# Kernel optimization log

Measured on AMD Instinct MI355X. Metric: run time of the kernel, lower is better.

Reference implementation:

```python
import jax, jax.numpy as jnp
import numpy as np

N_NODES = 100000
N_EDGES = 1600000
D_IN = 128
HID = 32
HEADS = 4
D_OUT = 40
NEG_SLOPE = 0.2


def edge_softmax(scores, dst, n_nodes):
    # scores: [E, H]; softmax over incoming edges of each destination node
    m = jax.ops.segment_max(scores, dst, num_segments=n_nodes)  # [N, H]
    e = jnp.exp(scores - m[dst])
    s = jax.ops.segment_sum(e, dst, num_segments=n_nodes)  # [N, H]
    return e / s[dst]


def gat_conv(x, src, dst, W, attn_l, attn_r, bias):
    # x: [N, Din]; W: [Din, H*F]; attn_l/attn_r: [H, F]; bias: [H*F]
    n = x.shape[0]
    h = (x @ W).reshape(n, HEADS, HID)          # [N, H, F]
    el = jnp.einsum('nhf,hf->nh', h, attn_l)    # [N, H]
    er = jnp.einsum('nhf,hf->nh', h, attn_r)    # [N, H]
    e = jax.nn.leaky_relu(el[src] + er[dst], NEG_SLOPE)  # [E, H]
    a = edge_softmax(e, dst, n)                 # [E, H]
    msg = h[src] * a[:, :, None]                # [E, H, F]
    out = jax.ops.segment_sum(msg, dst, num_segments=n)  # [N, H, F]
    return out + bias.reshape(HEADS, HID)


def setup_inputs() -> dict:
    key = jax.random.key(0)
    ks = jax.random.split(key, 12)
    x = jax.random.normal(ks[0], (N_NODES, D_IN), dtype=jnp.float32)
    src = jax.random.randint(ks[1], (N_EDGES,), 0, N_NODES, dtype=jnp.int32)
    dst = jax.random.randint(ks[2], (N_EDGES,), 0, N_NODES, dtype=jnp.int32)
    s = 0.05
    W1 = jax.random.normal(ks[3], (D_IN, HEADS * HID), dtype=jnp.float32) * s
    al1 = jax.random.normal(ks[4], (HEADS, HID), dtype=jnp.float32) * s
    ar1 = jax.random.normal(ks[5], (HEADS, HID), dtype=jnp.float32) * s
    b1 = jnp.zeros((HEADS * HID,), dtype=jnp.float32)
    W2 = jax.random.normal(ks[6], (HEADS * HID, HEADS * HID), dtype=jnp.float32) * s
    al2 = jax.random.normal(ks[7], (HEADS, HID), dtype=jnp.float32) * s
    ar2 = jax.random.normal(ks[8], (HEADS, HID), dtype=jnp.float32) * s
    b2 = jnp.zeros((HEADS * HID,), dtype=jnp.float32)
    Wout = jax.random.normal(ks[9], (HEADS * HID, D_OUT), dtype=jnp.float32) * s
    bout = jnp.zeros((D_OUT,), dtype=jnp.float32)
    return {"x": x, "src": src, "dst": dst,
            "W1": W1, "al1": al1, "ar1": ar1, "b1": b1,
            "W2": W2, "al2": al2, "ar2": ar2, "b2": b2,
            "Wout": Wout, "bout": bout}


def reference(x, src, dst, W1, al1, ar1, b1, W2, al2, ar2, b2, Wout, bout):
    n = x.shape[0]
    h = gat_conv(x, src, dst, W1, al1, ar1, b1).reshape(n, -1)  # flatten(1)
    h = jax.nn.elu(h)
    h = gat_conv(h, src, dst, W2, al2, ar2, b2).reshape(n, -1)
    h = jax.nn.elu(h)
    return h @ Wout + bout  # final Linear, flatten(1) is a no-op on 2D
```

## Files before the change

kernel.cpp:

```cpp
#include <hip/hip_runtime.h>
#include <hip/hip_fp16.h>
#include <math.h>

#define N_NODES 100000
#define N_EDGES 1600000
#define NEG_SLOPE 0.2f

#define NB ((N_NODES + 255) / 256)
#define NC 1024
#define CHUNK ((N_EDGES + NC - 1) / NC)

__device__ __forceinline__ float lrelu(float x) { return x > 0.f ? x : NEG_SLOPE * x; }
__device__ __forceinline__ float eluf(float x)  { return x > 0.f ? x : expm1f(x); }


__global__ __launch_bounds__(256) void p1_hist(const int* __restrict__ dst,
                                               int* __restrict__ H) {
  __shared__ int hist[NB];
  int c = blockIdx.x, t = threadIdx.x;
  for (int i = t; i < NB; i += 256) hist[i] = 0;
  __syncthreads();
  int e0 = c * CHUNK, e1 = min(e0 + CHUNK, N_EDGES);
  for (int e = e0 + t; e < e1; e += 256) atomicAdd(&hist[dst[e] >> 8], 1);
  __syncthreads();
  for (int i = t; i < NB; i += 256) H[i * NC + c] = hist[i];
}

__global__ __launch_bounds__(256) void p2_colscan(int* __restrict__ H,
                                                  int* __restrict__ colTotal) {
  __shared__ int sh[256];
  int b = blockIdx.x, t = threadIdx.x;
  int4 v = *(int4*)&H[b * NC + t * 4];
  int tsum = v.x + v.y + v.z + v.w;
  sh[t] = tsum;
  __syncthreads();
  for (int off = 1; off < 256; off <<= 1) {
    int u = (t >= off) ? sh[t - off] : 0;
    __syncthreads();
    sh[t] += u;
    __syncthreads();
  }
  int excl = sh[t] - tsum;
  int4 o;
  o.x = excl;
  o.y = excl + v.x;
  o.z = o.y + v.y;
  o.w = o.z + v.z;
  *(int4*)&H[b * NC + t * 4] = o;
  if (t == 255) colTotal[b] = sh[255];
}

__global__ __launch_bounds__(512) void p3_bucketscan(const int* __restrict__ colTotal,
                                                     int* __restrict__ bucketBase) {
  __shared__ int sh[512];
  int t = threadIdx.x;
  int v = (t < NB) ? colTotal[t] : 0;
  sh[t] = v;
  __syncthreads();
  for (int off = 1; off < 512; off <<= 1) {
    int u = (t >= off) ? sh[t - off] : 0;
    __syncthreads();
    sh[t] += u;
    __syncthreads();
  }
  if (t < NB) bucketBase[t] = sh[t] - v;
  if (t == NB - 1) bucketBase[NB] = sh[t];
}

__global__ __launch_bounds__(256) void p4_scatter(const int* __restrict__ src,
                                                  const int* __restrict__ dst,
                                                  const int* __restrict__ H,
                                                  const int* __restrict__ bucketBase,
                                                  int* __restrict__ tmp) {
  __shared__ int cur[NB];
  int c = blockIdx.x, t = threadIdx.x;
  for (int i = t; i < NB; i += 256) cur[i] = bucketBase[i] + H[i * NC + c];
  __syncthreads();
  int e0 = c * CHUNK, e1 = min(e0 + CHUNK, N_EDGES);
  for (int e = e0 + t; e < e1; e += 256) {
    int d = dst[e];
    int pos = atomicAdd(&cur[d >> 8], 1);
    tmp[pos] = (src[e] << 8) | (d & 255);
  }
}

__global__ __launch_bounds__(256) void p5_build(const int* __restrict__ tmp,
                                                const int* __restrict__ bucketBase,
                                                int* __restrict__ rowstart,
                                                int* __restrict__ csr_src) {
  __shared__ int hist[256];
  __shared__ int sh[256];
  __shared__ int cur[256];
  int b = blockIdx.x, t = threadIdx.x;
  int ebase = bucketBase[b], eend = bucketBase[b + 1];
  hist[t] = 0;
  __syncthreads();
  for (int e = ebase + t; e < eend; e += 256) atomicAdd(&hist[tmp[e] & 255], 1);
  __syncthreads();
  int v = hist[t];
  sh[t] = v;
  __syncthreads();
  for (int off = 1; off < 256; off <<= 1) {
    int u = (t >= off) ? sh[t - off] : 0;
    __syncthreads();
    sh[t] += u;
    __syncthreads();
  }
  int excl = sh[t] - v;
  int node = b * 256 + t;
  if (node < N_NODES) rowstart[node] = ebase + excl;
  cur[t] = excl;
  __syncthreads();
  for (int e = ebase + t; e < eend; e += 256) {
    int p = tmp[e];
    int pos = ebase + atomicAdd(&cur[p & 255], 1);
    csr_src[pos] = p >> 8;
  }
  if (b == 0 && t == 0) rowstart[N_NODES] = N_EDGES;
}

template <bool FP16IN>
__global__ __launch_bounds__(256) void gemm128_elr(const void* __restrict__ Av,
                                                   const float* __restrict__ W,
                                                   const float* __restrict__ al,
                                                   const float* __restrict__ ar,
                                                   __half* __restrict__ C,
                                                   float* __restrict__ el,
                                                   float* __restrict__ er, int N) {
  __shared__ float As[32 * 68];
  __shared__ float Ws[32 * 132];
  __shared__ float als[128], ars[128];
  int tid = threadIdx.x;
  int tx = tid & 15, ty = tid >> 4;
  int rowBase = blockIdx.x * 64;

  if (tid < 128) { als[tid] = al[tid]; ars[tid] = ar[tid]; }

  float acc0[4][4] = {};
  float acc1[4][4] = {};

  const float4* W4 = (const float4*)W;

  for (int kc = 0; kc < 128; kc += 32) {
    __syncthreads();
    if constexpr (FP16IN) {
      const __half* A = (const __half*)Av;
      int r = tid >> 2, c8 = (tid & 3) * 8;
      int gr = min(rowBase + r, N - 1);
      float4 raw = *(const float4*)&A[(size_t)gr * 128 + kc + c8];
      const __half2* hp = (const __half2*)&raw;
      float2 f0 = __half22float2(hp[0]);
      float2 f1 = __half22float2(hp[1]);
      float2 f2 = __half22float2(hp[2]);
      float2 f3 = __half22float2(hp[3]);
      As[(c8 + 0) * 68 + r] = f0.x; As[(c8 + 1) * 68 + r] = f0.y;
      As[(c8 + 2) * 68 + r] = f1.x; As[(c8 + 3) * 68 + r] = f1.y;
      As[(c8 + 4) * 68 + r] = f2.x; As[(c8 + 5) * 68 + r] = f2.y;
      As[(c8 + 6) * 68 + r] = f3.x; As[(c8 + 7) * 68 + r] = f3.y;
    } else {
      const float4* A4 = (const float4*)Av;
#pragma unroll
      for (int i = 0; i < 2; i++) {
        int v = tid + 256 * i;
        int r = v >> 3, c4 = v & 7;
        int gr = min(rowBase + r, N - 1);
        float4 val = A4[(size_t)gr * 32 + (kc >> 2) + c4];
        As[(c4 * 4 + 0) * 68 + r] = val.x;
        As[(c4 * 4 + 1) * 68 + r] = val.y;
        As[(c4 * 4 + 2) * 68 + r] = val.z;
        As[(c4 * 4 + 3) * 68 + r] = val.w;
      }
    }
#pragma unroll
    for (int i = 0; i < 4; i++) {
      int v = tid + 256 * i;
      int r = v >> 5, c4 = v & 31;
      float4 val = W4[(size_t)(kc + r) * 32 + c4];
      *(float4*)&Ws[r * 132 + c4 * 4] = val;
    }
    __syncthreads();

#pragma unroll 4
    for (int k = 0; k < 32; k++) {
      float4 a4 = *(const float4*)&As[k * 68 + ty * 4];
      float a[4] = {a4.x, a4.y, a4.z, a4.w};
      float4 w0 = *(const float4*)&Ws[k * 132 + tx * 4];
      float4 w1 = *(const float4*)&Ws[k * 132 + 64 + tx * 4];
#pragma unroll
      for (int i = 0; i < 4; i++) {
        acc0[i][0] = fmaf(a[i], w0.x, acc0[i][0]);
        acc0[i][1] = fmaf(a[i], w0.y, acc0[i][1]);
        acc0[i][2] = fmaf(a[i], w0.z, acc0[i][2]);
        acc0[i][3] = fmaf(a[i], w0.w, acc0[i][3]);
        acc1[i][0] = fmaf(a[i], w1.x, acc1[i][0]);
        acc1[i][1] = fmaf(a[i], w1.y, acc1[i][1]);
        acc1[i][2] = fmaf(a[i], w1.z, acc1[i][2]);
        acc1[i][3] = fmaf(a[i], w1.w, acc1[i][3]);
      }
    }
  }

  float alr0[4], arr0[4], alr1[4], arr1[4];
#pragma unroll
  for (int j = 0; j < 4; j++) {
    alr0[j] = als[4 * tx + j];      arr0[j] = ars[4 * tx + j];
    alr1[j] = als[64 + 4 * tx + j]; arr1[j] = ars[64 + 4 * tx + j];
  }
#pragma unroll
  for (int i = 0; i < 4; i++) {
    float pel0 = 0.f, per0 = 0.f, pel1 = 0.f, per1 = 0.f;
#pragma unroll
    for (int j = 0; j < 4; j++) {
      pel0 = fmaf(acc0[i][j], alr0[j], pel0);
      per0 = fmaf(acc0[i][j], arr0[j], per0);
      pel1 = fmaf(acc1[i][j], alr1[j], pel1);
      per1 = fmaf(acc1[i][j], arr1[j], per1);
    }
#pragma unroll
    for (int m = 1; m < 8; m <<= 1) {
      pel0 += __shfl_xor(pel0, m, 64);
      per0 += __shfl_xor(per0, m, 64);
      pel1 += __shfl_xor(pel1, m, 64);
      per1 += __shfl_xor(per1, m, 64);
    }
    int row = rowBase + ty * 4 + i;
    if (row < N) {
      __half2 p0 = __float22half2_rn(make_float2(acc0[i][0], acc0[i][1]));
      __half2 p1 = __float22half2_rn(make_float2(acc0[i][2], acc0[i][3]));
      __half2 q0 = __float22half2_rn(make_float2(acc1[i][0], acc1[i][1]));
      __half2 q1 = __float22half2_rn(make_float2(acc1[i][2], acc1[i][3]));
      float2 pk0, pk1;
      ((__half2*)&pk0)[0] = p0; ((__half2*)&pk0)[1] = p1;
      ((__half2*)&pk1)[0] = q0; ((__half2*)&pk1)[1] = q1;
      *(float2*)&C[(size_t)row * 128 + 4 * tx] = pk0;
      *(float2*)&C[(size_t)row * 128 + 64 + 4 * tx] = pk1;
      if ((tx & 7) == 0) {
        int hb = tx >> 3;
        el[row * 4 + hb] = pel0;     er[row * 4 + hb] = per0;
        el[row * 4 + 2 + hb] = pel1; er[row * 4 + 2 + hb] = per1;
      }
    }
  }
}

__global__ __launch_bounds__(256) void agg_fused(const __half* __restrict__ h,
                                                 const float* __restrict__ el,
                                                 const float* __restrict__ er,
                                                 const int* __restrict__ rowstart,
                                                 const int* __restrict__ csr_src,
                                                 const float* __restrict__ bias,
                                                 __half* __restrict__ out) {
  __shared__ float wlds[16][17][4];
  __shared__ int   ilds[16][17];
  int tid = threadIdx.x;
  int slot = tid >> 4;
  int l = tid & 15;
  int n = blockIdx.x * 16 + slot;
  if (n >= N_NODES) return;
  int base = rowstart[n];
  int deg = rowstart[n + 1] - base;
  int f0 = l * 8;
  int head = l >> 2;
  float acc[8] = {};
  float lsum = 0.f;

  if (deg > 0) {
    float4 erv = *(const float4*)&er[n * 4];

    for (int t0 = 0; t0 < deg; t0 += 16) {
      int e = t0 + l;
      bool act = e < deg;
      int s = act ? csr_src[base + e] : 0;
      float4 elv = *(const float4*)&el[s * 4];
      float w0 = act ? __expf(fminf(lrelu(elv.x + erv.x), 30.f)) : 0.f;
      float w1 = act ? __expf(fminf(lrelu(elv.y + erv.y), 30.f)) : 0.f;
      float w2 = act ? __expf(fminf(lrelu(elv.z + erv.z), 30.f)) : 0.f;
      float w3 = act ? __expf(fminf(lrelu(elv.w + erv.w), 30.f)) : 0.f;
      *(float4*)&wlds[slot][l][0] = make_float4(w0, w1, w2, w3);
      ilds[slot][l] = s;
      __builtin_amdgcn_wave_barrier();

      int nt = min(16, deg - t0);
#pragma unroll 4
      for (int i = 0; i < nt; i++) {
        int si = ilds[slot][i];
        float wi = wlds[slot][i][head];
        lsum += wi;
        float4 raw = *(const float4*)&h[(size_t)si * 128 + f0];
        const __half2* hp = (const __half2*)&raw;
        float2 c0 = __half22float2(hp[0]);
        float2 c1 = __half22float2(hp[1]);
        float2 c2 = __half22float2(hp[2]);
        float2 c3 = __half22float2(hp[3]);
        acc[0] = fmaf(c0.x, wi, acc[0]); acc[1] = fmaf(c0.y, wi, acc[1]);
        acc[2] = fmaf(c1.x, wi, acc[2]); acc[3] = fmaf(c1.y, wi, acc[3]);
        acc[4] = fmaf(c2.x, wi, acc[4]); acc[5] = fmaf(c2.y, wi, acc[5]);
        acc[6] = fmaf(c3.x, wi, acc[6]); acc[7] = fmaf(c3.y, wi, acc[7]);
      }
      __builtin_amdgcn_wave_barrier();
    }
    float rh = 1.f / lsum;
#pragma unroll
    for (int j = 0; j < 8; j++) acc[j] *= rh;
  }
  float4 b0 = *(const float4*)&bias[f0];
  float4 b1 = *(const float4*)&bias[f0 + 4];
  float r0 = eluf(acc[0] + b0.x), r1 = eluf(acc[1] + b0.y);
  float r2 = eluf(acc[2] + b0.z), r3 = eluf(acc[3] + b0.w);
  float r4 = eluf(acc[4] + b1.x), r5 = eluf(acc[5] + b1.y);
  float r6 = eluf(acc[6] + b1.z), r7 = eluf(acc[7] + b1.w);
  __half2 pk[4];
  pk[0] = __float22half2_rn(make_float2(r0, r1));
  pk[1] = __float22half2_rn(make_float2(r2, r3));
  pk[2] = __float22half2_rn(make_float2(r4, r5));
  pk[3] = __float22half2_rn(make_float2(r6, r7));
  *(float4*)&out[(size_t)n * 128 + f0] = *(float4*)pk;
}

__global__ __launch_bounds__(256) void gemm_out_k(const __half* __restrict__ A,
                                                  const float* __restrict__ Wo,
                                                  const float* __restrict__ bo,
                                                  float* __restrict__ C, int N) {
  __shared__ float As[64 * 132];
  __shared__ float Ws[128 * 44];
  int tid = threadIdx.x;
  int rowBase = blockIdx.x * 64;
  for (int i = tid; i < 128 * 40; i += 256) {
    int r = i / 40, c = i % 40;
    Ws[r * 44 + c] = Wo[i];
  }
#pragma unroll
  for (int j = 0; j < 4; j++) {
    int v = tid + 256 * j;
    int r = v >> 4, c8 = (v & 15) * 8;
    int gr = min(rowBase + r, N - 1);
    float4 raw = *(const float4*)&A[(size_t)gr * 128 + c8];
    const __half2* hp = (const __half2*)&raw;
    float2 f0 = __half22float2(hp[0]);
    float2 f1 = __half22float2(hp[1]);
    float2 f2 = __half22float2(hp[2]);
    float2 f3 = __half22float2(hp[3]);
    float* dstp = &As[r * 132 + c8];
    dstp[0] = f0.x; dstp[1] = f0.y; dstp[2] = f1.x; dstp[3] = f1.y;
    dstp[4] = f2.x; dstp[5] = f2.y; dstp[6] = f3.x; dstp[7] = f3.y;
  }
  __syncthreads();
  int rg = tid >> 4, cg = tid & 15;
  if (cg < 10) {
    float acc[4][4] = {};
#pragma unroll 4
    for (int k = 0; k < 128; k++) {
      float a[4];
#pragma unroll
      for (int i = 0; i < 4; i++) a[i] = As[(rg + 16 * i) * 132 + k];
      float4 w = *(const float4*)&Ws[k * 44 + cg * 4];
#pragma unroll
      for (int i = 0; i < 4; i++) {
        acc[i][0] = fmaf(a[i], w.x, acc[i][0]);
        acc[i][1] = fmaf(a[i], w.y, acc[i][1]);
        acc[i][2] = fmaf(a[i], w.z, acc[i][2]);
        acc[i][3] = fmaf(a[i], w.w, acc[i][3]);
      }
    }
    float4 bv = *(const float4*)&bo[cg * 4];
#pragma unroll
    for (int i = 0; i < 4; i++) {
      int r = rowBase + rg + 16 * i;
      if (r < N) {
        float4 o = make_float4(acc[i][0] + bv.x, acc[i][1] + bv.y,
                               acc[i][2] + bv.z, acc[i][3] + bv.w);
        *(float4*)&C[r * 40 + cg * 4] = o;
      }
    }
  }
}

extern "C" void kernel_launch(void* const* d_in, const int* in_sizes, int n_in,
                              void* d_out, int out_size, void* d_ws, size_t ws_size,
                              hipStream_t stream) {
  const float* x    = (const float*)d_in[0];
  const int*   src  = (const int*)d_in[1];
  const int*   dst  = (const int*)d_in[2];
  const float* W1   = (const float*)d_in[3];
  const float* al1  = (const float*)d_in[4];
  const float* ar1  = (const float*)d_in[5];
  const float* b1   = (const float*)d_in[6];
  const float* W2   = (const float*)d_in[7];
  const float* al2  = (const float*)d_in[8];
  const float* ar2  = (const float*)d_in[9];
  const float* b2   = (const float*)d_in[10];
  const float* Wout = (const float*)d_in[11];
  const float* bout = (const float*)d_in[12];
  float* out = (float*)d_out;

  const int N = N_NODES, E = N_EDGES;
  size_t off = 0;
  auto alloc = [&](size_t bytes) {
    void* p = (char*)d_ws + off;
    off += (bytes + 255) & ~(size_t)255;
    return p;
  };
  __half* hh  = (__half*)alloc((size_t)N * 128 * 2);
  __half* o16 = (__half*)alloc((size_t)N * 128 * 2);
  float* el  = (float*)alloc((size_t)N * 4 * 4);
  float* er  = (float*)alloc((size_t)N * 4 * 4);
  int* rowstart   = (int*)alloc((size_t)(N + 1) * 4);
  int* H          = (int*)alloc((size_t)NB * NC * 4);
  int* colTotal   = (int*)alloc((size_t)NB * 4);
  int* bucketBase = (int*)alloc((size_t)(NB + 1) * 4);
  int* tmp        = (int*)alloc((size_t)E * 4);
  int* csr_src    = (int*)alloc((size_t)E * 4);
  (void)ws_size; (void)in_sizes; (void)n_in; (void)out_size;

  p1_hist<<<NC, 256, 0, stream>>>(dst, H);
  p2_colscan<<<NB, 256, 0, stream>>>(H, colTotal);
  p3_bucketscan<<<1, 512, 0, stream>>>(colTotal, bucketBase);
  p4_scatter<<<NC, 256, 0, stream>>>(src, dst, H, bucketBase, tmp);
  p5_build<<<NB, 256, 0, stream>>>(tmp, bucketBase, rowstart, csr_src);

  int gemmGrid = (N + 63) / 64;
  int outGrid  = (N + 63) / 64;
  int aggGrid  = (N + 15) / 16;

  gemm128_elr<false><<<gemmGrid, 256, 0, stream>>>(x, W1, al1, ar1, hh, el, er, N);
  agg_fused<<<aggGrid, 256, 0, stream>>>(hh, el, er, rowstart, csr_src, b1, o16);

  gemm128_elr<true><<<gemmGrid, 256, 0, stream>>>(o16, W2, al2, ar2, hh, el, er, N);
  agg_fused<<<aggGrid, 256, 0, stream>>>(hh, el, er, rowstart, csr_src, b2, o16);

  gemm_out_k<<<outGrid, 256, 0, stream>>>(o16, Wout, bout, out, N);
}
```

Before: 324.5 us.

## Replace FMA-tiled 128x128 GEMMs with fp16 MFMA kernel staging output through LDS

The two node-feature GEMMs (x@W1 and h@W2) move from a scalar-FMA register-tiled kernel to one built on the 16x16x16 fp16 MFMA instruction. Each block transposes the whole W into LDS as fp16 and each wave loads its A fragments straight into registers. The el/er attention dot products are reduced with shuffles from the MFMA accumulator layout, and the fp16 output tile is staged through LDS for coalesced stores. This cuts ALU time in the GEMMs, but the first layer's fp32 input is now rounded to fp16, and every block re-converts W from global memory.

```diff
diff --git a/kernel.cpp b/kernel.cpp
--- a/kernel.cpp
+++ b/kernel.cpp
@@ -9,6 +9,15 @@
 #define NB ((N_NODES + 255) / 256)
 #define NC 1024
 #define CHUNK ((N_EDGES + NC - 1) / NC)
+
+#define WT_STRIDE 136
+#define CS_STRIDE 136
+
+typedef _Float16 f16x2 __attribute__((ext_vector_type(2)));
+typedef _Float16 f16x4 __attribute__((ext_vector_type(4)));
+typedef float f32x4v __attribute__((ext_vector_type(4)));
+
+#define MFMA16(a, b, c) __builtin_amdgcn_mfma_f32_16x16x16f16(a, b, c, 0, 0, 0)
 
 __device__ __forceinline__ float lrelu(float x) { return x > 0.f ? x : NEG_SLOPE * x; }
 __device__ __forceinline__ float eluf(float x)  { return x > 0.f ? x : expm1f(x); }
@@ -120,125 +129,111 @@
 }
 
 template <bool FP16IN>
-__global__ __launch_bounds__(256) void gemm128_elr(const void* __restrict__ Av,
-                                                   const float* __restrict__ W,
-                                                   const float* __restrict__ al,
-                                                   const float* __restrict__ ar,
-                                                   __half* __restrict__ C,
-                                                   float* __restrict__ el,
-                                                   float* __restrict__ er, int N) {
-  __shared__ float As[32 * 68];
-  __shared__ float Ws[32 * 132];
+__global__ __launch_bounds__(256) void gemm128_mfma(const void* __restrict__ Av,
+                                                    const float* __restrict__ W,
+                                                    const float* __restrict__ al,
+                                                    const float* __restrict__ ar,
+                                                    __half* __restrict__ C,
+                                                    float* __restrict__ el,
+                                                    float* __restrict__ er, int N) {
+  __shared__ _Float16 WtCs[128 * WT_STRIDE];
   __shared__ float als[128], ars[128];
   int tid = threadIdx.x;
-  int tx = tid & 15, ty = tid >> 4;
+  int wv = tid >> 6;
+  int l = tid & 63;
+  int li = l & 15, lk = l >> 4;
   int rowBase = blockIdx.x * 64;
 
   if (tid < 128) { als[tid] = al[tid]; ars[tid] = ar[tid]; }
 
-  float acc0[4][4] = {};
-  float acc1[4][4] = {};
-
-  const float4* W4 = (const float4*)W;
-
-  for (int kc = 0; kc < 128; kc += 32) {
-    __syncthreads();
-    if constexpr (FP16IN) {
-      const __half* A = (const __half*)Av;
-      int r = tid >> 2, c8 = (tid & 3) * 8;
-      int gr = min(rowBase + r, N - 1);
-      float4 raw = *(const float4*)&A[(size_t)gr * 128 + kc + c8];
-      const __half2* hp = (const __half2*)&raw;
-      float2 f0 = __half22float2(hp[0]);
-      float2 f1 = __half22float2(hp[1]);
-      float2 f2 = __half22float2(hp[2]);
-      float2 f3 = __half22float2(hp[3]);
-      As[(c8 + 0) * 68 + r] = f0.x; As[(c8 + 1) * 68 + r] = f0.y;
-      As[(c8 + 2) * 68 + r] = f1.x; As[(c8 + 3) * 68 + r] = f1.y;
-      As[(c8 + 4) * 68 + r] = f2.x; As[(c8 + 5) * 68 + r] = f2.y;
-      As[(c8 + 6) * 68 + r] = f3.x; As[(c8 + 7) * 68 + r] = f3.y;
-    } else {
-      const float4* A4 = (const float4*)Av;
-#pragma unroll
-      for (int i = 0; i < 2; i++) {
-        int v = tid + 256 * i;
-        int r = v >> 3, c4 = v & 7;
-        int gr = min(rowBase + r, N - 1);
-        float4 val = A4[(size_t)gr * 32 + (kc >> 2) + c4];
-        As[(c4 * 4 + 0) * 68 + r] = val.x;
-        As[(c4 * 4 + 1) * 68 + r] = val.y;
-        As[(c4 * 4 + 2) * 68 + r] = val.z;
-        As[(c4 * 4 + 3) * 68 + r] = val.w;
+#pragma unroll 4
+  for (int i = 0; i < 32; i++) {
+    int idx = tid + 256 * i;
+    int c = idx & 127, k = (idx >> 7) * 2;
+    f16x2 p;
+    p[0] = (_Float16)W[k * 128 + c];
+    p[1] = (_Float16)W[(k + 1) * 128 + c];
+    *(f16x2*)&WtCs[c * WT_STRIDE + k] = p;
+  }
+
+  f16x4 afr[8];
+  int ra = min(rowBase + wv * 16 + li, N - 1);
+  if constexpr (FP16IN) {
+    const _Float16* A = (const _Float16*)Av;
+#pragma unroll
+    for (int ch = 0; ch < 8; ch++)
+      afr[ch] = *(const f16x4*)&A[(size_t)ra * 128 + ch * 16 + lk * 4];
+  } else {
+    const float* A = (const float*)Av;
+#pragma unroll
+    for (int ch = 0; ch < 8; ch++) {
+      float4 v = *(const float4*)&A[(size_t)ra * 128 + ch * 16 + lk * 4];
+      f16x4 a;
+      a[0] = (_Float16)v.x; a[1] = (_Float16)v.y;
+      a[2] = (_Float16)v.z; a[3] = (_Float16)v.w;
+      afr[ch] = a;
+    }
+  }
+  __syncthreads();
+
+  f32x4v acc[8];
+#pragma unroll
+  for (int ct = 0; ct < 8; ct++) acc[ct] = (f32x4v){0.f, 0.f, 0.f, 0.f};
+
+#pragma unroll
+  for (int ch = 0; ch < 8; ch++) {
+#pragma unroll
+    for (int ct = 0; ct < 8; ct++) {
+      f16x4 b = *(const f16x4*)&WtCs[(ct * 16 + li) * WT_STRIDE + ch * 16 + lk * 4];
+      acc[ct] = MFMA16(afr[ch], b, acc[ct]);
+    }
+  }
+
+  float alc[8], arc[8];
+#pragma unroll
+  for (int ct = 0; ct < 8; ct++) {
+    alc[ct] = als[ct * 16 + li];
+    arc[ct] = ars[ct * 16 + li];
+  }
+#pragma unroll
+  for (int j = 0; j < 4; j++) {
+    float el4[4], er4[4];
+#pragma unroll
+    for (int hh = 0; hh < 4; hh++) {
+      el4[hh] = acc[2 * hh][j] * alc[2 * hh] + acc[2 * hh + 1][j] * alc[2 * hh + 1];
+      er4[hh] = acc[2 * hh][j] * arc[2 * hh] + acc[2 * hh + 1][j] * arc[2 * hh + 1];
+    }
+#pragma unroll
+    for (int m = 1; m < 16; m <<= 1) {
+#pragma unroll
+      for (int hh = 0; hh < 4; hh++) {
+        el4[hh] += __shfl_xor(el4[hh], m, 64);
+        er4[hh] += __shfl_xor(er4[hh], m, 64);
       }
     }
-#pragma unroll
-    for (int i = 0; i < 4; i++) {
-      int v = tid + 256 * i;
-      int r = v >> 5, c4 = v & 31;
-      float4 val = W4[(size_t)(kc + r) * 32 + c4];
-      *(float4*)&Ws[r * 132 + c4 * 4] = val;
-    }
-    __syncthreads();
-
-#pragma unroll 4
-    for (int k = 0; k < 32; k++) {
-      float4 a4 = *(const float4*)&As[k * 68 + ty * 4];
-      float a[4] = {a4.x, a4.y, a4.z, a4.w};
-      float4 w0 = *(const float4*)&Ws[k * 132 + tx * 4];
-      float4 w1 = *(const float4*)&Ws[k * 132 + 64 + tx * 4];
-#pragma unroll
-      for (int i = 0; i < 4; i++) {
-        acc0[i][0] = fmaf(a[i], w0.x, acc0[i][0]);
-        acc0[i][1] = fmaf(a[i], w0.y, acc0[i][1]);
-        acc0[i][2] = fmaf(a[i], w0.z, acc0[i][2]);
-        acc0[i][3] = fmaf(a[i], w0.w, acc0[i][3]);
-        acc1[i][0] = fmaf(a[i], w1.x, acc1[i][0]);
-        acc1[i][1] = fmaf(a[i], w1.y, acc1[i][1]);
-        acc1[i][2] = fmaf(a[i], w1.z, acc1[i][2]);
-        acc1[i][3] = fmaf(a[i], w1.w, acc1[i][3]);
-      }
-    }
-  }
-
-  float alr0[4], arr0[4], alr1[4], arr1[4];
+    int row = rowBase + wv * 16 + lk * 4 + j;
+    if (li == 0 && row < N) {
+      *(float4*)&el[row * 4] = make_float4(el4[0], el4[1], el4[2], el4[3]);
+      *(float4*)&er[row * 4] = make_float4(er4[0], er4[1], er4[2], er4[3]);
+    }
+  }
+
+  __syncthreads();
 #pragma unroll
   for (int j = 0; j < 4; j++) {
-    alr0[j] = als[4 * tx + j];      arr0[j] = ars[4 * tx + j];
-    alr1[j] = als[64 + 4 * tx + j]; arr1[j] = ars[64 + 4 * tx + j];
-  }
-#pragma unroll
-  for (int i = 0; i < 4; i++) {
-    float pel0 = 0.f, per0 = 0.f, pel1 = 0.f, per1 = 0.f;
-#pragma unroll
-    for (int j = 0; j < 4; j++) {
-      pel0 = fmaf(acc0[i][j], alr0[j], pel0);
-      per0 = fmaf(acc0[i][j], arr0[j], per0);
-      pel1 = fmaf(acc1[i][j], alr1[j], pel1);
-      per1 = fmaf(acc1[i][j], arr1[j], per1);
-    }
-#pragma unroll
-    for (int m = 1; m < 8; m <<= 1) {
-      pel0 += __shfl_xor(pel0, m, 64);
-      per0 += __shfl_xor(per0, m, 64);
-      pel1 += __shfl_xor(pel1, m, 64);
-      per1 += __shfl_xor(per1, m, 64);
-    }
-    int row = rowBase + ty * 4 + i;
-    if (row < N) {
-      __half2 p0 = __float22half2_rn(make_float2(acc0[i][0], acc0[i][1]));
-      __half2 p1 = __float22half2_rn(make_float2(acc0[i][2], acc0[i][3]));
-      __half2 q0 = __float22half2_rn(make_float2(acc1[i][0], acc1[i][1]));
-      __half2 q1 = __float22half2_rn(make_float2(acc1[i][2], acc1[i][3]));
-      float2 pk0, pk1;
-      ((__half2*)&pk0)[0] = p0; ((__half2*)&pk0)[1] = p1;
-      ((__half2*)&pk1)[0] = q0; ((__half2*)&pk1)[1] = q1;
-      *(float2*)&C[(size_t)row * 128 + 4 * tx] = pk0;
-      *(float2*)&C[(size_t)row * 128 + 64 + 4 * tx] = pk1;
-      if ((tx & 7) == 0) {
-        int hb = tx >> 3;
-        el[row * 4 + hb] = pel0;     er[row * 4 + hb] = per0;
-        el[row * 4 + 2 + hb] = pel1; er[row * 4 + 2 + hb] = per1;
-      }
+    int rl = wv * 16 + lk * 4 + j;
+#pragma unroll
+    for (int ct = 0; ct < 8; ct++)
+      WtCs[rl * CS_STRIDE + ct * 16 + li] = (_Float16)acc[ct][j];
+  }
+  __syncthreads();
+  int rrow = tid >> 2, ckk = tid & 3;
+  int grow = rowBase + rrow;
+  if (grow < N) {
+#pragma unroll
+    for (int q = 0; q < 4; q++) {
+      float4 v = *(float4*)&WtCs[rrow * CS_STRIDE + ckk * 32 + q * 8];
+      *(float4*)&C[(size_t)grow * 128 + ckk * 32 + q * 8] = v;
     }
   }
 }
@@ -422,10 +417,10 @@
   int outGrid  = (N + 63) / 64;
   int aggGrid  = (N + 15) / 16;
 
-  gemm128_elr<false><<<gemmGrid, 256, 0, stream>>>(x, W1, al1, ar1, hh, el, er, N);
+  gemm128_mfma<false><<<gemmGrid, 256, 0, stream>>>(x, W1, al1, ar1, hh, el, er, N);
   agg_fused<<<aggGrid, 256, 0, stream>>>(hh, el, er, rowstart, csr_src, b1, o16);
 
-  gemm128_elr<true><<<gemmGrid, 256, 0, stream>>>(o16, W2, al2, ar2, hh, el, er, N);
+  gemm128_mfma<true><<<gemmGrid, 256, 0, stream>>>(o16, W2, al2, ar2, hh, el, er, N);
   agg_fused<<<aggGrid, 256, 0, stream>>>(hh, el, er, rowstart, csr_src, b2, o16);
 
   gemm_out_k<<<outGrid, 256, 0, stream>>>(o16, Wout, bout, out, N);
```

New measurement: 283.3 us. 1.15x faster.
